# Optimization experiments

Hardware: AMD Instinct MI355X
Metric: run time of the kernel (lower is better)

Reference implementation:

```python
import jax, jax.numpy as jnp
import numpy as np

NUM_HEADS, KEY_DIM, BLOCK, HALO = 8, 64, 8, 4
KV_KERNEL = BLOCK + 2 * HALO  # 16
EMB = NUM_HEADS * KEY_DIM     # 512


def setup_inputs() -> dict:
    key = jax.random.key(0)
    k = jax.random.split(key, 6)
    stddev = KEY_DIM ** -0.5
    return {
        "x": jax.random.normal(k[0], (8, 64, 64, 512), jnp.float32),
        "wq": jax.random.normal(k[1], (512, EMB), jnp.float32) * 0.02,
        "wkv": jax.random.normal(k[2], (512, 2 * EMB), jnp.float32) * 0.02,
        "wout": jax.random.normal(k[3], (EMB, EMB), jnp.float32) * 0.02,
        "pos_w": jax.random.normal(k[4], (KEY_DIM, 2 * KV_KERNEL - 1), jnp.float32) * stddev,
        "pos_h": jax.random.normal(k[5], (KEY_DIM, 2 * KV_KERNEL - 1), jnp.float32) * stddev,
    }


def rel_to_abs(rel):
    # rel: [B, N, hh, ww, 2*pos_dim-1] -> [B, N, hh, ww, pos_dim]
    b, n, hh, ww, dim = rel.shape
    pos_dim = (dim + 1) // 2
    gap = pos_dim - ww
    flat = rel.reshape(b, n, hh, ww * dim)[:, :, :, ww - 1:-1]
    return flat.reshape(b, n, hh, ww, 2 * (pos_dim - 1))[:, :, :, :, gap:pos_dim + gap]


def halo_forward(x, wq, wkv, wout, pos_w, pos_h):
    B, H, W, C = x.shape
    h, w = H // BLOCK, W // BLOCK
    K = KV_KERNEL
    scale = 1.0 / jnp.sqrt(jnp.asarray(KEY_DIM, x.dtype))

    # Query: [B, hd, h, w, block^2, key_dim]
    q = (x @ wq) * scale
    q = q.reshape(B, h, BLOCK, w, BLOCK, NUM_HEADS, KEY_DIM)
    attn_q = q.transpose(0, 5, 1, 3, 2, 4, 6).reshape(B, NUM_HEADS, h, w, BLOCK * BLOCK, KEY_DIM)

    # Overlapping halo KV windows (im2col-style gather, like tf.image.extract_patches)
    kv = x @ wkv
    kv_p = jnp.pad(kv, ((0, 0), (HALO, HALO), (HALO, HALO), (0, 0)))
    idx_h = jnp.arange(h)[:, None] * BLOCK + jnp.arange(K)[None, :]  # [h, K]
    idx_w = jnp.arange(w)[:, None] * BLOCK + jnp.arange(K)[None, :]  # [w, K]
    patches = kv_p[:, idx_h][:, :, :, idx_w]          # [B, h, K, w, K, 2*EMB]
    patches = patches.transpose(0, 1, 3, 2, 4, 5)     # [B, h, w, K, K, 2*EMB]
    patches = patches.reshape(B, h, w, K * K, NUM_HEADS, 2 * KEY_DIM)
    patches = patches.transpose(0, 4, 1, 2, 3, 5)     # [B, hd, h, w, K^2, 2*key_dim]
    key_t, val = patches[..., :KEY_DIM], patches[..., KEY_DIM:]

    scores = jnp.einsum('bnhwqc,bnhwkc->bnhwqk', attn_q, key_t)  # [B,hd,h,w,bq,bk]

    # Relative position logits (width + height), query already carries qk_scale
    pos_q = attn_q.reshape(B, NUM_HEADS * h * w, BLOCK, BLOCK, KEY_DIM)
    rel_w = rel_to_abs(pos_q @ pos_w)                                      # [B,N,hb,wb,K]
    rel_h = rel_to_abs(pos_q.transpose(0, 1, 3, 2, 4) @ pos_h)
    rel_h = rel_h.transpose(0, 1, 3, 2, 4)                                 # [B,N,hb,wb,K]
    pos = rel_w[..., None, :] + rel_h[..., :, None]                        # [B,N,hb,wb,Kh,Kw]
    pos = pos.reshape(B, NUM_HEADS, h, w, BLOCK * BLOCK, K * K)

    attn = jax.nn.softmax(scores + pos, axis=-1)
    out = jnp.einsum('bnhwqk,bnhwkc->bnhwqc', attn, val)
    out = out.reshape(B, NUM_HEADS, h, w, BLOCK, BLOCK, KEY_DIM)
    out = out.transpose(0, 2, 4, 3, 5, 1, 6).reshape(B, H, W, EMB)
    return out @ wout


def reference(x, wq, wkv, wout, pos_w, pos_h):
    return halo_forward(x, wq, wkv, wout, pos_w, pos_h)
```

## Files before the change

kernel.cpp:

```cpp
#include <hip/hip_runtime.h>
#include <hip/hip_fp16.h>
#include <math.h>

typedef _Float16 f16x8 __attribute__((ext_vector_type(8)));
typedef _Float16 f16x4 __attribute__((ext_vector_type(4)));
typedef float    f32x4 __attribute__((ext_vector_type(4)));

#define M_TOT 32768
#define VROW  4608

__device__ __forceinline__ void gload16(const void* g, void* l) {
    __builtin_amdgcn_global_load_lds(
        (const __attribute__((address_space(1))) unsigned int*)g,
        (__attribute__((address_space(3))) unsigned int*)l, 16, 0, 0);
}

__device__ __forceinline__ f32x4 mfma32(f16x8 a, f16x8 b, f32x4 c) {
    return __builtin_amdgcn_mfma_f32_16x16x32_f16(a, b, c, 0, 0, 0);
}

__global__ __launch_bounds__(256) void conv_x(const float* __restrict__ x,
                                              __half* __restrict__ y) {
    const size_t i = ((size_t)blockIdx.x * 256 + threadIdx.x) * 8;
    float4 a = *(const float4*)&x[i];
    float4 b = *(const float4*)&x[i + 4];
    __half2 h[4];
    h[0] = __floats2half2_rn(a.x, a.y);
    h[1] = __floats2half2_rn(a.z, a.w);
    h[2] = __floats2half2_rn(b.x, b.y);
    h[3] = __floats2half2_rn(b.z, b.w);
    *(float4*)&y[i] = *(float4*)h;
}

__global__ __launch_bounds__(256) void conv_w(const float* __restrict__ wq,
                                              const float* __restrict__ wkv,
                                              const float* __restrict__ wout,
                                              __half* __restrict__ wT,
                                              __half* __restrict__ woT) {
    const int id = blockIdx.x * 256 + threadIdx.x;
    const int nr = id >> 9, k = id & 511;
    if (nr < 512) {
        wT[(size_t)nr * 512 + k]  = __float2half(wq[k * 512 + nr] * 0.125f);
    } else if (nr < 1536) {
        wT[(size_t)nr * 512 + k]  = __float2half(wkv[k * 1024 + (nr - 512)]);
    } else {
        woT[(size_t)(nr - 1536) * 512 + k] = __float2half(wout[k * 512 + (nr - 1536)]);
    }
}

__global__ __launch_bounds__(256) void pos_prep(const float* __restrict__ posw,
                                                const float* __restrict__ posh,
                                                __half* __restrict__ posT) {
    const int id = blockIdx.x * 256 + threadIdx.x;
    const int tb = id >> 11, idx = (id >> 6) & 31, d = id & 63;
    const float* src = tb ? posh : posw;
    posT[id] = __float2half((idx < 31) ? src[d * 31 + idx] : 0.f);
}

__global__ __launch_bounds__(256) void vborder(__half* __restrict__ vTp) {
    const int id = blockIdx.x * 256 + threadIdx.x;
    const int row = id >> 7, rem = id & 127;
    const int y = rem >> 1, side = rem & 1;
    f16x4 z = {(_Float16)0.f, (_Float16)0.f, (_Float16)0.f, (_Float16)0.f};
    *(f16x4*)(vTp + (size_t)row * VROW + y * 72 + side * 68) = z;
}

template <int MODE, int NBN>
__global__ __launch_bounds__(256) void mfma_gemm(
    const __half* __restrict__ A, const __half* __restrict__ Bt,
    __half* __restrict__ q16, __half* __restrict__ k16, __half* __restrict__ vTp,
    float* __restrict__ outf)
{
    __shared__ _Float16 As[128 * 32];
    __shared__ _Float16 Bs[128 * 32];

    const int t = threadIdx.x;
    const int l = t & 63, w = t >> 6;
    const int wr = w >> 1, wc = w & 1;

    const int bid = blockIdx.x;
    const int xcd = bid & 7, loc = bid >> 3;
    const int bm  = xcd * 32 + (loc & 31);
    const int bn  = loc >> 5;

    f32x4 zero = {0.f, 0.f, 0.f, 0.f};
    f32x4 acc[4][4];
    #pragma unroll
    for (int i = 0; i < 4; ++i)
        #pragma unroll
        for (int j = 0; j < 4; ++j) acc[i][j] = zero;

    const int srow = w * 32 + (l >> 2);
    const int sch  = (l & 3) * 8;
    const size_t abase = (size_t)(bm * 128 + srow) * 512 + sch;
    const size_t bbase = (size_t)(bn * 128 + srow) * 512 + sch;
    _Float16* ldsA0 = &As[(w * 2 + 0) * 512];
    _Float16* ldsA1 = &As[(w * 2 + 1) * 512];
    _Float16* ldsB0 = &Bs[(w * 2 + 0) * 512];
    _Float16* ldsB1 = &Bs[(w * 2 + 1) * 512];

    const int lr = l & 15, lk = (l >> 4) * 8;

    for (int k0 = 0; k0 < 512; k0 += 32) {
        gload16(A  + abase + k0,            ldsA0);
        gload16(A  + abase + 16 * 512 + k0, ldsA1);
        gload16(Bt + bbase + k0,            ldsB0);
        gload16(Bt + bbase + 16 * 512 + k0, ldsB1);
        __syncthreads();

        f16x8 af[4], bf[4];
        #pragma unroll
        for (int i = 0; i < 4; ++i)
            af[i] = *(const f16x8*)&As[(wr * 64 + i * 16 + lr) * 32 + lk];
        #pragma unroll
        for (int j = 0; j < 4; ++j)
            bf[j] = *(const f16x8*)&Bs[(wc * 64 + j * 16 + lr) * 32 + lk];
        #pragma unroll
        for (int i = 0; i < 4; ++i)
            #pragma unroll
            for (int j = 0; j < 4; ++j)
                acc[i][j] = mfma32(af[i], bf[j], acc[i][j]);
        __syncthreads();
    }

    const int lq = l >> 4;
    #pragma unroll
    for (int i = 0; i < 4; ++i) {
        #pragma unroll
        for (int j = 0; j < 4; ++j) {
            const int row0 = bm * 128 + wr * 64 + i * 16 + lq * 4;
            const int col  = bn * 128 + wc * 64 + j * 16 + lr;
            if (MODE == 1) {
                #pragma unroll
                for (int r = 0; r < 4; ++r)
                    outf[(size_t)(row0 + r) * 512 + col] = acc[i][j][r];
            } else if (bn < 4) {
                #pragma unroll
                for (int r = 0; r < 4; ++r)
                    q16[(size_t)(row0 + r) * 512 + col] = __float2half(acc[i][j][r]);
            } else if (wc == 0) {
                const int head = bn - 4, d2 = j * 16 + lr;
                #pragma unroll
                for (int r = 0; r < 4; ++r)
                    k16[(size_t)(row0 + r) * 512 + head * 64 + d2] = __float2half(acc[i][j][r]);
            } else {
                const int head = bn - 4, d2 = j * 16 + lr;
                const int bb = row0 >> 12, pix = row0 & 4095;
                const int py = pix >> 6, px = pix & 63;
                f16x4 pv;
                #pragma unroll
                for (int r = 0; r < 4; ++r) pv[r] = (_Float16)acc[i][j][r];
                *(f16x4*)(vTp + ((size_t)((bb * 8 + head) * 64 + d2)) * VROW + py * 72 + px + 4) = pv;
            }
        }
    }
}

__global__ __launch_bounds__(256, 3) void halo_attn(
    const __half* __restrict__ qbuf, const __half* __restrict__ kbuf,
    const __half* __restrict__ vTp, const __half* __restrict__ posT,
    const __half* __restrict__ zp, __half* __restrict__ obuf)
{
    __shared__ __align__(16) char KP[64 * 520];
    __shared__ float RWT[32][68];
    __shared__ float RHT[32][68];
    __shared__ float red[4][64];
    __shared__ float red2[4][64];

    const int hw = blockIdx.x;
    const int wg = (hw & 7) * 512 + (hw >> 3);
    const int wb = wg & 7, hb = (wg >> 3) & 7, n = (wg >> 6) & 7, b = wg >> 9;
    const int t = threadIdx.x;
    const int l = t & 63, g = t >> 6;
    const int hi = l >> 4, c15 = l & 15;

    #pragma unroll
    for (int it = 0; it < 8; ++it) {
        const int cid = it * 256 + t;
        const int S = cid * 16;
        const int row = S >> 7;
        const int d0h = (((S & 127) >> 4) ^ (row & 7)) * 8;
        const int ky = hb * 8 - 4 + (row >> 4);
        const int kx = wb * 8 - 4 + (row & 15);
        const bool ok = ((unsigned)ky < 64u) && ((unsigned)kx < 64u);
        const __half* src = ok ? (kbuf + ((size_t)((b * 64 + ky) * 64 + kx)) * 512 + n * 64 + d0h)
                               : zp;
        gload16(src, KP + (it * 256 + g * 64) * 16);
    }

    f16x8 vfrag[8];
    {
        const __half* vrow = vTp + ((size_t)((b * 8 + n) * 64 + g * 16 + c15)) * VROW;
        const int xoff = wb * 8 + (hi & 1) * 8;
        #pragma unroll
        for (int kc = 0; kc < 8; ++kc) {
            const int ki = kc * 2 + (hi >> 1);
            const int y = hb * 8 - 4 + ki;
            const __half* p = ((unsigned)y < 64u) ? (vrow + y * 72 + xoff) : zp;
            vfrag[kc] = *(const f16x8*)p;
        }
    }

    f16x8 qreg[4][2];
    #pragma unroll
    for (int qf = 0; qf < 4; ++qf) {
        const int q = qf * 16 + c15;
        const size_t pix = (size_t)((b * 64 + hb * 8 + (q >> 3)) * 64 + wb * 8 + (q & 7));
        #pragma unroll
        for (int dc = 0; dc < 2; ++dc)
            qreg[qf][dc] = *(const f16x8*)(qbuf + pix * 512 + n * 64 + dc * 32 + hi * 8);
    }

    {
        const int tb = g >> 1, ih = g & 1;
        f32x4 accp[4];
        #pragma unroll
        for (int qf = 0; qf < 4; ++qf) accp[qf] = (f32x4){0.f, 0.f, 0.f, 0.f};
        #pragma unroll
        for (int dc = 0; dc < 2; ++dc) {
            const f16x8 a = *(const f16x8*)(posT + tb * 2048 + (ih * 16 + c15) * 64 + dc * 32 + hi * 8);
            #pragma unroll
            for (int qf = 0; qf < 4; ++qf)
                accp[qf] = mfma32(a, qreg[qf][dc], accp[qf]);
        }
        float (*dst)[68] = tb ? RHT : RWT;
        #pragma unroll
        for (int qf = 0; qf < 4; ++qf)
            #pragma unroll
            for (int r = 0; r < 4; ++r)
                dst[ih * 16 + hi * 4 + r][qf * 16 + c15] = accp[qf][r];
    }
    __syncthreads();

    f32x4 accs[4][4];
    #pragma unroll
    for (int kf = 0; kf < 4; ++kf)
        #pragma unroll
        for (int qf = 0; qf < 4; ++qf) accs[kf][qf] = (f32x4){0.f, 0.f, 0.f, 0.f};

    __builtin_amdgcn_s_setprio(1);
    #pragma unroll
    for (int kf = 0; kf < 4; ++kf) {
        const int row = g * 64 + kf * 16 + c15;
        #pragma unroll
        for (int dc = 0; dc < 2; ++dc) {
            const int off = (row * 128 + dc * 64 + hi * 16) ^ ((row & 7) << 4);
            f16x8 a = *(const f16x8*)(KP + off);
            #pragma unroll
            for (int qf = 0; qf < 4; ++qf)
                accs[kf][qf] = mfma32(a, qreg[qf][dc], accs[kf][qf]);
        }
    }
    __builtin_amdgcn_s_setprio(0);

    float mq[4];
    #pragma unroll
    for (int qf = 0; qf < 4; ++qf) {
        const int q = qf * 16 + c15;
        const int qj = q & 7, qi = q >> 3;
        float pa[4], pb[4];
        #pragma unroll
        for (int r = 0; r < 4; ++r)  pa[r] = RWT[hi * 4 + r - qj + 15][q];
        #pragma unroll
        for (int kf = 0; kf < 4; ++kf) pb[kf] = RHT[g * 4 + kf - qi + 15][q];
        float mm = -1e30f;
        #pragma unroll
        for (int kf = 0; kf < 4; ++kf)
            #pragma unroll
            for (int r = 0; r < 4; ++r) {
                const float s = accs[kf][qf][r] + pa[r] + pb[kf];
                accs[kf][qf][r] = s;
                mm = fmaxf(mm, s);
            }
        mm = fmaxf(mm, __shfl_xor(mm, 16));
        mm = fmaxf(mm, __shfl_xor(mm, 32));
        mq[qf] = mm;
    }
    if (l < 16) {
        #pragma unroll
        for (int qf = 0; qf < 4; ++qf) red[g][qf * 16 + l] = mq[qf];
    }
    __syncthreads();

    float sums[4];
    #pragma unroll
    for (int qf = 0; qf < 4; ++qf) {
        const int q = qf * 16 + c15;
        const float mfull = fmaxf(fmaxf(red[0][q], red[1][q]), fmaxf(red[2][q], red[3][q]));
        float ss = 0.f;
        #pragma unroll
        for (int kf = 0; kf < 4; ++kf)
            #pragma unroll
            for (int r = 0; r < 4; ++r) {
                const float p = __expf(accs[kf][qf][r] - mfull);
                accs[kf][qf][r] = p;
                ss += p;
            }
        ss += __shfl_xor(ss, 16);
        ss += __shfl_xor(ss, 32);
        sums[qf] = ss;
        #pragma unroll
        for (int kf = 0; kf < 4; ++kf) {
            __half2 h01 = __floats2half2_rn(accs[kf][qf][0], accs[kf][qf][1]);
            __half2 h23 = __floats2half2_rn(accs[kf][qf][2], accs[kf][qf][3]);
            uint2 wv;
            wv.x = *(unsigned*)&h01;
            wv.y = *(unsigned*)&h23;
            *(uint2*)(KP + q * 520 + (g * 64 + kf * 16 + hi * 4) * 2) = wv;
        }
    }
    if (l < 16) {
        #pragma unroll
        for (int qf = 0; qf < 4; ++qf) red2[g][qf * 16 + l] = sums[qf];
    }
    __syncthreads();

    f32x4 acco[4];
    #pragma unroll
    for (int qf = 0; qf < 4; ++qf) acco[qf] = (f32x4){0.f, 0.f, 0.f, 0.f};
    __builtin_amdgcn_s_setprio(1);
    #pragma unroll
    for (int kc = 0; kc < 8; ++kc) {
        const f16x8 bf = vfrag[kc];
        #pragma unroll
        for (int qf = 0; qf < 4; ++qf) {
            const char* pp = KP + (qf * 16 + c15) * 520 + kc * 64 + hi * 16;
            const f16x4 p0 = *(const f16x4*)pp;
            const f16x4 p1 = *(const f16x4*)(pp + 8);
            const f16x8 af = __builtin_shufflevector(p0, p1, 0, 1, 2, 3, 4, 5, 6, 7);
            acco[qf] = mfma32(af, bf, acco[qf]);
        }
    }
    __builtin_amdgcn_s_setprio(0);

    #pragma unroll
    for (int qf = 0; qf < 4; ++qf) {
        #pragma unroll
        for (int r = 0; r < 4; ++r) {
            const int q = qf * 16 + hi * 4 + r;
            const float den = red2[0][q] + red2[1][q] + red2[2][q] + red2[3][q];
            const float v = acco[qf][r] / den;
            const size_t pix = (size_t)((b * 64 + hb * 8 + (q >> 3)) * 64 + wb * 8 + (q & 7));
            obuf[pix * 512 + n * 64 + g * 16 + c15] = __float2half(v);
        }
    }
}

extern "C" void kernel_launch(void* const* d_in, const int* in_sizes, int n_in,
                              void* d_out, int out_size, void* d_ws, size_t ws_size,
                              hipStream_t stream)
{
    const float* x    = (const float*)d_in[0];
    const float* wq   = (const float*)d_in[1];
    const float* wkv  = (const float*)d_in[2];
    const float* wout = (const float*)d_in[3];
    const float* posw = (const float*)d_in[4];
    const float* posh = (const float*)d_in[5];
    float* out = (float*)d_out;

    const size_t NPIX = (size_t)M_TOT * 512;
    const size_t NVTP = (size_t)64 * 64 * VROW;
    __half* x16  = (__half*)d_ws;
    __half* wT   = x16 + NPIX;
    __half* woT  = wT + (size_t)1536 * 512;
    __half* q16  = woT + (size_t)512 * 512;
    __half* k16  = q16 + NPIX;
    __half* vTp  = k16 + NPIX;
    __half* o16  = vTp + NVTP;
    __half* zp   = o16 + NPIX;
    __half* posT = zp + 128;

    hipMemsetAsync(zp, 0, 256, stream);

    conv_x<<<(M_TOT * 512) / (256 * 8), 256, 0, stream>>>(x, x16);
    conv_w<<<(2048 * 512) / 256, 256, 0, stream>>>(wq, wkv, wout, wT, woT);
    pos_prep<<<16, 256, 0, stream>>>(posw, posh, posT);
    vborder<<<2048, 256, 0, stream>>>(vTp);

    mfma_gemm<0, 12><<<3072, 256, 0, stream>>>(x16, wT, q16, k16, vTp, nullptr);

    halo_attn<<<4096, 256, 0, stream>>>(q16, k16, vTp, posT, zp, o16);

    mfma_gemm<1, 4><<<1024, 256, 0, stream>>>(o16, woT, nullptr, nullptr, nullptr, out);
}
```

Measured before the change: 206.2 us.

## Double GEMM K-tile to 64 and XOR-swizzle LDS layout for bank-conflict-free reads

The projection GEMM now stages a 64-wide K slice per iteration instead of 32, halving the number of barrier-separated loop trips. The LDS tiles use 128-byte rows with an XOR swizzle of the 16-byte chunk index by row, so the MFMA fragment reads avoid bank conflicts. This costs twice the LDS per block, which may lower occupancy, and adds some address arithmetic. An unused scid_row array is left in the code.

```diff
diff --git a/kernel.cpp b/kernel.cpp
--- a/kernel.cpp
+++ b/kernel.cpp
@@ -71,59 +71,69 @@
     __half* __restrict__ q16, __half* __restrict__ k16, __half* __restrict__ vTp,
     float* __restrict__ outf)
 {
-    __shared__ _Float16 As[128 * 32];
-    __shared__ _Float16 Bs[128 * 32];
+    __shared__ __align__(16) char As[128 * 128];
+    __shared__ __align__(16) char Bs[128 * 128];
 
     const int t = threadIdx.x;
     const int l = t & 63, w = t >> 6;
     const int wr = w >> 1, wc = w & 1;
+    const int lr = l & 15, hi = l >> 4;
 
     const int bid = blockIdx.x;
     const int xcd = bid & 7, loc = bid >> 3;
     const int bm  = xcd * 32 + (loc & 31);
     const int bn  = loc >> 5;
 
-    f32x4 zero = {0.f, 0.f, 0.f, 0.f};
     f32x4 acc[4][4];
     #pragma unroll
     for (int i = 0; i < 4; ++i)
         #pragma unroll
-        for (int j = 0; j < 4; ++j) acc[i][j] = zero;
-
-    const int srow = w * 32 + (l >> 2);
-    const int sch  = (l & 3) * 8;
-    const size_t abase = (size_t)(bm * 128 + srow) * 512 + sch;
-    const size_t bbase = (size_t)(bn * 128 + srow) * 512 + sch;
-    _Float16* ldsA0 = &As[(w * 2 + 0) * 512];
-    _Float16* ldsA1 = &As[(w * 2 + 1) * 512];
-    _Float16* ldsB0 = &Bs[(w * 2 + 0) * 512];
-    _Float16* ldsB1 = &Bs[(w * 2 + 1) * 512];
-
-    const int lr = l & 15, lk = (l >> 4) * 8;
-
-    for (int k0 = 0; k0 < 512; k0 += 32) {
-        gload16(A  + abase + k0,            ldsA0);
-        gload16(A  + abase + 16 * 512 + k0, ldsA1);
-        gload16(Bt + bbase + k0,            ldsB0);
-        gload16(Bt + bbase + 16 * 512 + k0, ldsB1);
+        for (int j = 0; j < 4; ++j) acc[i][j] = (f32x4){0.f, 0.f, 0.f, 0.f};
+
+    const int scid_row[4] = { (t * 16) >> 7, (256 * 16 + t * 16) >> 7,
+                              (512 * 16 + t * 16) >> 7, (768 * 16 + t * 16) >> 7 };
+    const int sch = (t & 7);
+
+    for (int k0 = 0; k0 < 512; k0 += 64) {
+        #pragma unroll
+        for (int it = 0; it < 4; ++it) {
+            const int row = it * 32 + (t >> 3);
+            const int kk  = k0 + ((sch ^ (row & 7)) * 8);
+            gload16(A + (size_t)(bm * 128 + row) * 512 + kk,
+                    As + (it * 256 + w * 64) * 16);
+        }
+        #pragma unroll
+        for (int it = 0; it < 4; ++it) {
+            const int row = it * 32 + (t >> 3);
+            const int kk  = k0 + ((sch ^ (row & 7)) * 8);
+            gload16(Bt + (size_t)(bn * 128 + row) * 512 + kk,
+                    Bs + (it * 256 + w * 64) * 16);
+        }
         __syncthreads();
 
-        f16x8 af[4], bf[4];
-        #pragma unroll
-        for (int i = 0; i < 4; ++i)
-            af[i] = *(const f16x8*)&As[(wr * 64 + i * 16 + lr) * 32 + lk];
-        #pragma unroll
-        for (int j = 0; j < 4; ++j)
-            bf[j] = *(const f16x8*)&Bs[(wc * 64 + j * 16 + lr) * 32 + lk];
-        #pragma unroll
-        for (int i = 0; i < 4; ++i)
-            #pragma unroll
-            for (int j = 0; j < 4; ++j)
-                acc[i][j] = mfma32(af[i], bf[j], acc[i][j]);
+        #pragma unroll
+        for (int dc = 0; dc < 2; ++dc) {
+            f16x8 af[4], bf[4];
+            #pragma unroll
+            for (int i = 0; i < 4; ++i) {
+                const int ra = wr * 64 + i * 16 + lr;
+                af[i] = *(const f16x8*)(As + ra * 128 + (((dc * 4 + hi) ^ (ra & 7)) * 16));
+            }
+            #pragma unroll
+            for (int j = 0; j < 4; ++j) {
+                const int rb = wc * 64 + j * 16 + lr;
+                bf[j] = *(const f16x8*)(Bs + rb * 128 + (((dc * 4 + hi) ^ (rb & 7)) * 16));
+            }
+            #pragma unroll
+            for (int i = 0; i < 4; ++i)
+                #pragma unroll
+                for (int j = 0; j < 4; ++j)
+                    acc[i][j] = mfma32(af[i], bf[j], acc[i][j]);
+        }
         __syncthreads();
     }
 
-    const int lq = l >> 4;
+    const int lq = hi;
     #pragma unroll
     for (int i = 0; i < 4; ++i) {
         #pragma unroll
```

Result: slower. 211.4 us (+2.5%).
